# Optimization experiments

Measured on AMD Instinct MI355X. Metric: run time of the kernel, lower is better.

The kernel has to match this reference:

```python
import jax, jax.numpy as jnp
import numpy as np

B, S, E, H, F = 8, 1024, 1024, 16, 4096
D = E // H  # head_dim = 64
EPS = 1e-5


def setup_inputs() -> dict:
    key = jax.random.key(0)
    ks = jax.random.split(key, 12)
    s = 0.02
    return {
        "x": jax.random.normal(ks[0], (B, S, E), dtype=jnp.float32),
        # per-head projections (shared across heads), torch stores [out,in]; we use [in,out]
        "Wq": jax.random.normal(ks[1], (D, D), dtype=jnp.float32) * s,
        "Wk": jax.random.normal(ks[2], (D, D), dtype=jnp.float32) * s,
        "Wv": jax.random.normal(ks[3], (D, D), dtype=jnp.float32) * s,
        "Wo": jax.random.normal(ks[4], (E, E), dtype=jnp.float32) * s,
        "bo": jnp.zeros((E,), dtype=jnp.float32),
        "W1": jax.random.normal(ks[5], (E, F), dtype=jnp.float32) * s,
        "b1": jnp.zeros((F,), dtype=jnp.float32),
        "W2": jax.random.normal(ks[6], (F, E), dtype=jnp.float32) * s,
        "b2": jnp.zeros((E,), dtype=jnp.float32),
        "g1": jnp.ones((E,), dtype=jnp.float32),
        "beta1": jnp.zeros((E,), dtype=jnp.float32),
        "g2": jnp.ones((E,), dtype=jnp.float32),
        "beta2": jnp.zeros((E,), dtype=jnp.float32),
    }


def _layer_norm(x, g, b):
    m = jnp.mean(x, axis=-1, keepdims=True)
    v = jnp.mean(jnp.square(x - m), axis=-1, keepdims=True)
    return (x - m) * jax.lax.rsqrt(v + EPS) * g + b


def reference(x, Wq, Wk, Wv, Wo, bo, W1, b1, W2, b2, g1, beta1, g2, beta2):
    b, s, e = x.shape
    # --- attention sublayer (pre-norm) ---
    nx = _layer_norm(x, g1, beta1)
    h = nx.reshape(b, s, H, D)              # [B,S,H,D]
    q = h @ Wq                               # per-head linear, weight shared over heads
    k = h @ Wk
    v = h @ Wv
    energy = jnp.einsum('bqhd,bkhd->bhqk', q, k)  # full [B,H,S,S] scores
    mask = jnp.tril(jnp.ones((s, s), dtype=bool))
    energy = jnp.where(mask, energy, -jnp.inf)
    att = jax.nn.softmax(energy / jnp.sqrt(jnp.float32(e)), axis=-1)  # NOTE: scale by sqrt(embed_dim)
    o = jnp.einsum('bhqk,bkhd->bqhd', att, v).reshape(b, s, e)
    x = x + (o @ Wo + bo)
    # --- MLP sublayer (pre-norm); dropout is identity in eval ---
    nx = _layer_norm(x, g2, beta2)
    x = x + (jax.nn.relu(nx @ W1 + b1) @ W2 + b2)
    return x
```

## Files before the change

kernel.cpp:

```cpp
#include <hip/hip_runtime.h>

typedef unsigned short u16;
typedef __attribute__((ext_vector_type(4))) float f4;
typedef __attribute__((ext_vector_type(8))) short s8v;
typedef __attribute__((ext_vector_type(4))) unsigned short u16x4;

#define DEVINL __device__ __forceinline__

DEVINL float b2f(u16 u) { union { unsigned i; float f; } x; x.i = ((unsigned)u) << 16; return x.f; }
DEVINL u16 f2b(float f) {
  union { float f; unsigned i; } x; x.f = f;
  unsigned r = 0x7FFFu + ((x.i >> 16) & 1u);
  return (u16)((x.i + r) >> 16);
}

#define GLD_LDS16(g, l)                                                        \
  __builtin_amdgcn_global_load_lds((__attribute__((address_space(1))) void*)(g), \
                                   (__attribute__((address_space(3))) void*)(l), 16, 0, 0)

__global__ __launch_bounds__(256) void k_transpose(const float* __restrict__ in,
                                                   u16* __restrict__ out, int R, int C) {
  __shared__ float t[32][33];
  int tx = threadIdx.x & 31, ty = threadIdx.x >> 5;
  int c0 = blockIdx.x * 32, r0 = blockIdx.y * 32;
#pragma unroll
  for (int i = 0; i < 32; i += 8)
    t[ty + i][tx] = in[(long)(r0 + ty + i) * C + (c0 + tx)];
  __syncthreads();
#pragma unroll
  for (int i = 0; i < 32; i += 8)
    out[(long)(c0 + ty + i) * R + (r0 + tx)] = f2b(t[tx][ty + i]);
}

__global__ __launch_bounds__(256) void k_vtrans(const u16* __restrict__ v, u16* __restrict__ vt) {
  __shared__ u16 t[64][72];
  int bh = blockIdx.x, b = bh >> 4, h = bh & 15;
  int s0 = blockIdx.y * 64;
  int tid = threadIdx.x;
#pragma unroll
  for (int p = 0; p < 2; ++p) {
    int idx = p * 256 + tid;
    int sl = idx >> 3, c8 = (idx & 7) * 8;
    *(s8v*)(&t[sl][c8]) = *(const s8v*)(v + (((long)(b * 1024 + s0 + sl) * 16 + h) * 64) + c8);
  }
  __syncthreads();
#pragma unroll
  for (int p = 0; p < 2; ++p) {
    int idx = p * 256 + tid;
    int d = idx >> 3, c8 = (idx & 7) * 8;
    s8v o;
#pragma unroll
    for (int e = 0; e < 8; ++e) o[e] = (short)t[c8 + e][d];
    *(s8v*)(vt + ((long)bh * 64 + d) * 1024 + s0 + c8) = o;
  }
}

__global__ __launch_bounds__(256) void k_layernorm(const float* __restrict__ x,
                                                   const float* __restrict__ g,
                                                   const float* __restrict__ be,
                                                   u16* __restrict__ out) {
  long row = blockIdx.x;
  int tid = threadIdx.x;
  f4 v = ((const f4*)(x + row * 1024))[tid];
  float s = v[0] + v[1] + v[2] + v[3];
  float s2 = v[0] * v[0] + v[1] * v[1] + v[2] * v[2] + v[3] * v[3];
#pragma unroll
  for (int off = 32; off > 0; off >>= 1) {
    s += __shfl_down(s, off, 64);
    s2 += __shfl_down(s2, off, 64);
  }
  __shared__ float red[8];
  int wv = tid >> 6, ln = tid & 63;
  if (ln == 0) { red[wv] = s; red[4 + wv] = s2; }
  __syncthreads();
  s = red[0] + red[1] + red[2] + red[3];
  s2 = red[4] + red[5] + red[6] + red[7];
  float mean = s * (1.0f / 1024.0f);
  float var = s2 * (1.0f / 1024.0f) - mean * mean;
  float rs = rsqrtf(var + 1e-5f);
  f4 gg = ((const f4*)g)[tid];
  f4 bb = ((const f4*)be)[tid];
  u16x4 o;
#pragma unroll
  for (int i = 0; i < 4; ++i) o[i] = f2b((v[i] - mean) * rs * gg[i] + bb[i]);
  ((u16x4*)(out + row * 1024))[tid] = o;
}

__global__ __launch_bounds__(256) void k_qkv(const u16* __restrict__ nx, const u16* __restrict__ WqT,
                                             const u16* __restrict__ WkT, const u16* __restrict__ WvT,
                                             u16* __restrict__ q, u16* __restrict__ k,
                                             u16* __restrict__ v) {
  int tid = threadIdx.x, lane = tid & 63, wave = tid >> 6;
  int quad = lane >> 4, l16 = lane & 15;
  long rbase = (long)blockIdx.x * 64 + wave * 16;
  s8v a0 = *(const s8v*)(nx + (rbase + l16) * 64 + quad * 8);
  s8v a1 = *(const s8v*)(nx + (rbase + l16) * 64 + 32 + quad * 8);
  const u16* Ws[3] = {WqT, WkT, WvT};
  u16* Os[3] = {q, k, v};
#pragma unroll
  for (int t = 0; t < 3; ++t) {
#pragma unroll
    for (int j = 0; j < 4; ++j) {
      s8v b0 = *(const s8v*)(Ws[t] + (j * 16 + l16) * 64 + quad * 8);
      s8v b1 = *(const s8v*)(Ws[t] + (j * 16 + l16) * 64 + 32 + quad * 8);
      f4 acc = {0.f, 0.f, 0.f, 0.f};
      acc = __builtin_amdgcn_mfma_f32_16x16x32_bf16(a0, b0, acc, 0, 0, 0);
      acc = __builtin_amdgcn_mfma_f32_16x16x32_bf16(a1, b1, acc, 0, 0, 0);
#pragma unroll
      for (int r = 0; r < 4; ++r)
        Os[t][(rbase + quad * 4 + r) * 64 + j * 16 + l16] = f2b(acc[r]);
    }
  }
}

__global__ __launch_bounds__(256) void k_attn_mfma(const u16* __restrict__ q,
                                                   const u16* __restrict__ kk,
                                                   const u16* __restrict__ vt,
                                                   u16* __restrict__ o) {
  constexpr int LDK = 72;
  __shared__ u16 Ks[64 * LDK];
  __shared__ u16 Vt[64 * LDK];
  __shared__ u16 Ps[4][16 * LDK];
  int tid = threadIdx.x, lane = tid & 63, wave = tid >> 6;
  int quad = lane >> 4, l16 = lane & 15;
  int b = blockIdx.x >> 4, h = blockIdx.x & 15;
  int qi = (int)gridDim.y - 1 - (int)blockIdx.y;
  int q0 = qi * 64 + wave * 16;

  const u16* qp = q + (((long)(b * 1024 + q0 + l16)) * 16 + h) * 64;
  s8v aq0 = *(const s8v*)(qp + quad * 8);
  s8v aq1 = *(const s8v*)(qp + 32 + quad * 8);

  f4 O[4];
  float m_[4], l_[4];
#pragma unroll
  for (int jd = 0; jd < 4; ++jd) O[jd] = f4{0.f, 0.f, 0.f, 0.f};
#pragma unroll
  for (int r = 0; r < 4; ++r) { m_[r] = -__builtin_inff(); l_[r] = 0.f; }

  for (int kt = 0; kt <= qi; ++kt) {
    __syncthreads();
#pragma unroll
    for (int p = 0; p < 2; ++p) {
      int idx = p * 256 + tid;
      int row = idx >> 3, c8 = (idx & 7) * 8;
      *(s8v*)(Ks + row * LDK + c8) =
          *(const s8v*)(kk + (((long)(b * 1024 + kt * 64 + row)) * 16 + h) * 64 + c8);
      *(s8v*)(Vt + row * LDK + c8) =
          *(const s8v*)(vt + ((long)blockIdx.x * 64 + row) * 1024 + kt * 64 + c8);
    }
    __syncthreads();

    f4 sf[4];
#pragma unroll
    for (int jn = 0; jn < 4; ++jn) {
      s8v b0 = *(const s8v*)(Ks + (jn * 16 + l16) * LDK + quad * 8);
      s8v b1 = *(const s8v*)(Ks + (jn * 16 + l16) * LDK + 32 + quad * 8);
      f4 acc = f4{0.f, 0.f, 0.f, 0.f};
      acc = __builtin_amdgcn_mfma_f32_16x16x32_bf16(aq0, b0, acc, 0, 0, 0);
      acc = __builtin_amdgcn_mfma_f32_16x16x32_bf16(aq1, b1, acc, 0, 0, 0);
      sf[jn] = acc;
    }
    bool diag = (kt == qi);
    float rm[4];
#pragma unroll
    for (int r = 0; r < 4; ++r) rm[r] = -__builtin_inff();
#pragma unroll
    for (int jn = 0; jn < 4; ++jn)
#pragma unroll
      for (int r = 0; r < 4; ++r) {
        float v = sf[jn][r] * 0.03125f;
        if (diag && (jn * 16 + l16 > wave * 16 + quad * 4 + r)) v = -__builtin_inff();
        sf[jn][r] = v;
        rm[r] = fmaxf(rm[r], v);
      }
#pragma unroll
    for (int off = 1; off < 16; off <<= 1)
#pragma unroll
      for (int r = 0; r < 4; ++r) rm[r] = fmaxf(rm[r], __shfl_xor(rm[r], off, 64));
    float alpha[4], rs[4];
#pragma unroll
    for (int r = 0; r < 4; ++r) {
      float mn = fmaxf(m_[r], rm[r]);
      alpha[r] = __expf(m_[r] - mn);
      m_[r] = mn;
      rs[r] = 0.f;
    }
#pragma unroll
    for (int jn = 0; jn < 4; ++jn)
#pragma unroll
      for (int r = 0; r < 4; ++r) {
        float p = __expf(sf[jn][r] - m_[r]);
        rs[r] += p;
        Ps[wave][(quad * 4 + r) * LDK + jn * 16 + l16] = f2b(p);
      }
#pragma unroll
    for (int off = 1; off < 16; off <<= 1)
#pragma unroll
      for (int r = 0; r < 4; ++r) rs[r] += __shfl_xor(rs[r], off, 64);
#pragma unroll
    for (int r = 0; r < 4; ++r) l_[r] = l_[r] * alpha[r] + rs[r];
#pragma unroll
    for (int jd = 0; jd < 4; ++jd)
#pragma unroll
      for (int r = 0; r < 4; ++r) O[jd][r] *= alpha[r];
    asm volatile("s_waitcnt lgkmcnt(0)" ::: "memory");
    s8v p0 = *(const s8v*)(&Ps[wave][l16 * LDK + quad * 8]);
    s8v p1 = *(const s8v*)(&Ps[wave][l16 * LDK + 32 + quad * 8]);
#pragma unroll
    for (int jd = 0; jd < 4; ++jd) {
      s8v b0 = *(const s8v*)(Vt + (jd * 16 + l16) * LDK + quad * 8);
      s8v b1 = *(const s8v*)(Vt + (jd * 16 + l16) * LDK + 32 + quad * 8);
      O[jd] = __builtin_amdgcn_mfma_f32_16x16x32_bf16(p0, b0, O[jd], 0, 0, 0);
      O[jd] = __builtin_amdgcn_mfma_f32_16x16x32_bf16(p1, b1, O[jd], 0, 0, 0);
    }
  }
#pragma unroll
  for (int r = 0; r < 4; ++r) {
    float inv = 1.0f / l_[r];
    u16* op = o + (((long)(b * 1024 + q0 + quad * 4 + r)) * 16 + h) * 64;
#pragma unroll
    for (int jd = 0; jd < 4; ++jd) op[jd * 16 + l16] = f2b(O[jd][r] * inv);
  }
}

template <int EPI>
__global__ __launch_bounds__(256) void k_gemm_bt(const u16* __restrict__ A, const u16* __restrict__ BT,
                                                 const float* __restrict__ bias,
                                                 const float* __restrict__ resid,
                                                 void* __restrict__ outp, int M, int N, int K) {
  __shared__ u16 sA[2][128 * 32];
  __shared__ u16 sB[2][128 * 32];
  int tid = threadIdx.x, lane = tid & 63, wave = tid >> 6;
  int quad = lane >> 4, l16 = lane & 15;
  int wm = wave >> 1, wn = wave & 1;
  long bm = blockIdx.x, bn = blockIdx.y;
  int srow = tid >> 2, scol = (tid & 3) * 8;
  const u16* ga = A + (bm * 128 + srow) * (long)K + scol;
  const u16* gb = BT + (bn * 128 + srow) * (long)K + scol;
  int woff = wave * 1024;

  f4 acc[4][4];
#pragma unroll
  for (int i = 0; i < 4; ++i)
#pragma unroll
    for (int j = 0; j < 4; ++j) acc[i][j] = f4{0.f, 0.f, 0.f, 0.f};

  {
    char* lA = (char*)&sA[0][0] + woff;
    char* lB = (char*)&sB[0][0] + woff;
    GLD_LDS16(ga, lA);
    GLD_LDS16(ga + 64 * (long)K, lA + 4096);
    GLD_LDS16(gb, lB);
    GLD_LDS16(gb + 64 * (long)K, lB + 4096);
  }

  for (int k0 = 0; k0 < K; k0 += 32) {
    int cur = (k0 >> 5) & 1;
    __syncthreads();
    int k1 = k0 + 32;
    if (k1 < K) {
      char* lA = (char*)&sA[cur ^ 1][0] + woff;
      char* lB = (char*)&sB[cur ^ 1][0] + woff;
      GLD_LDS16(ga + k1, lA);
      GLD_LDS16(ga + 64 * (long)K + k1, lA + 4096);
      GLD_LDS16(gb + k1, lB);
      GLD_LDS16(gb + 64 * (long)K + k1, lB + 4096);
    }
    const u16* cA = sA[cur];
    const u16* cB = sB[cur];
    s8v aF[4], bF[4];
#pragma unroll
    for (int i = 0; i < 4; ++i)
      aF[i] = *(const s8v*)(cA + (wm * 64 + i * 16 + l16) * 32 + quad * 8);
#pragma unroll
    for (int j = 0; j < 4; ++j)
      bF[j] = *(const s8v*)(cB + (wn * 64 + j * 16 + l16) * 32 + quad * 8);
#pragma unroll
    for (int i = 0; i < 4; ++i)
#pragma unroll
      for (int j = 0; j < 4; ++j)
        acc[i][j] = __builtin_amdgcn_mfma_f32_16x16x32_bf16(aF[i], bF[j], acc[i][j], 0, 0, 0);
  }

#pragma unroll
  for (int i = 0; i < 4; ++i) {
#pragma unroll
    for (int j = 0; j < 4; ++j) {
      long row = bm * 128 + wm * 64 + i * 16 + quad * 4;
      int col = (int)bn * 128 + wn * 64 + j * 16 + l16;
      float bcol = bias[col];
#pragma unroll
      for (int r = 0; r < 4; ++r) {
        float val = acc[i][j][r] + bcol;
        if (EPI == 1) {
          ((u16*)outp)[(row + r) * (long)N + col] = f2b(val > 0.f ? val : 0.f);
        } else {
          ((float*)outp)[(row + r) * (long)N + col] = resid[(row + r) * (long)N + col] + val;
        }
      }
    }
  }
}

extern "C" void kernel_launch(void* const* d_in, const int* in_sizes, int n_in, void* d_out,
                              int out_size, void* d_ws, size_t ws_size, hipStream_t stream) {
  const float* x = (const float*)d_in[0];
  const float* Wq = (const float*)d_in[1];
  const float* Wk = (const float*)d_in[2];
  const float* Wv = (const float*)d_in[3];
  const float* Wo = (const float*)d_in[4];
  const float* bo = (const float*)d_in[5];
  const float* W1 = (const float*)d_in[6];
  const float* b1 = (const float*)d_in[7];
  const float* W2 = (const float*)d_in[8];
  const float* b2 = (const float*)d_in[9];
  const float* g1 = (const float*)d_in[10];
  const float* be1 = (const float*)d_in[11];
  const float* g2 = (const float*)d_in[12];
  const float* be2 = (const float*)d_in[13];

  char* ws = (char*)d_ws;
  const size_t MB = 1ull << 20;
  u16* nx = (u16*)(ws + 0);
  u16* qb = (u16*)(ws + 16 * MB);
  u16* kb = (u16*)(ws + 32 * MB);
  u16* vb = (u16*)(ws + 48 * MB);
  float* x1 = (float*)(ws + 64 * MB);
  u16* h1 = (u16*)(ws + 96 * MB);
  u16* vtr = (u16*)(ws + 96 * MB);
  u16* WoT = (u16*)(ws + 160 * MB);
  u16* W1T = (u16*)(ws + 162 * MB);
  u16* W2T = (u16*)(ws + 170 * MB);
  u16* WqT = (u16*)(ws + 178 * MB);
  u16* WkT = WqT + 64 * 64;
  u16* WvT = WkT + 64 * 64;
  u16* ob = nx;
  u16* nx2 = qb;

  k_transpose<<<dim3(32, 32), 256, 0, stream>>>(Wo, WoT, 1024, 1024);
  k_transpose<<<dim3(128, 32), 256, 0, stream>>>(W1, W1T, 1024, 4096);
  k_transpose<<<dim3(32, 128), 256, 0, stream>>>(W2, W2T, 4096, 1024);
  k_transpose<<<dim3(2, 2), 256, 0, stream>>>(Wq, WqT, 64, 64);
  k_transpose<<<dim3(2, 2), 256, 0, stream>>>(Wk, WkT, 64, 64);
  k_transpose<<<dim3(2, 2), 256, 0, stream>>>(Wv, WvT, 64, 64);

  k_layernorm<<<8192, 256, 0, stream>>>(x, g1, be1, nx);
  k_qkv<<<2048, 256, 0, stream>>>(nx, WqT, WkT, WvT, qb, kb, vb);
  k_vtrans<<<dim3(128, 16), 256, 0, stream>>>(vb, vtr);
  k_attn_mfma<<<dim3(128, 16), 256, 0, stream>>>(qb, kb, vtr, ob);
  k_gemm_bt<2><<<dim3(64, 8), 256, 0, stream>>>(ob, WoT, bo, x, x1, 8192, 1024, 1024);

  k_layernorm<<<8192, 256, 0, stream>>>(x1, g2, be2, nx2);
  k_gemm_bt<1><<<dim3(64, 32), 256, 0, stream>>>(nx2, W1T, b1, nullptr, h1, 8192, 4096, 1024);
  k_gemm_bt<2><<<dim3(64, 8), 256, 0, stream>>>(h1, W2T, b2, x1, d_out, 8192, 1024, 4096);
}
```

Baseline: 457.2 us.

## Split K across two wave groups per block for N=1024 GEMMs

Adds a 512-thread GEMM kernel in which two groups of four waves each handle half of the K dimension for the same 128x128 output tile. Their partial accumulators are summed through LDS before the bias and residual epilogue. It replaces the Wo and W2 projections, whose 512-block grids leave the GPU's CUs under-occupied with waves. The cost is double the LDS (64KB) and an extra reduction and sync step.

```diff
diff --git a/kernel.cpp b/kernel.cpp
--- a/kernel.cpp
+++ b/kernel.cpp
@@ -297,6 +297,97 @@
           ((u16*)outp)[(row + r) * (long)N + col] = f2b(val > 0.f ? val : 0.f);
         } else {
           ((float*)outp)[(row + r) * (long)N + col] = resid[(row + r) * (long)N + col] + val;
+        }
+      }
+    }
+  }
+}
+
+template <int EPI>
+__global__ __launch_bounds__(512) void k_gemm_sk(const u16* __restrict__ A, const u16* __restrict__ BT,
+                                                 const float* __restrict__ bias,
+                                                 const float* __restrict__ resid,
+                                                 void* __restrict__ outp, int M, int N, int K) {
+  __shared__ char smem[65536];
+  int tid = threadIdx.x;
+  int grp = tid >> 8, gt = tid & 255;
+  int lane = tid & 63, w4 = (tid >> 6) & 3;
+  int quad = lane >> 4, l16 = lane & 15;
+  int wm = w4 >> 1, wn = w4 & 1;
+  long bm = blockIdx.x, bn = blockIdx.y;
+  int srow = gt >> 2, scol = (gt & 3) * 8;
+  int Kh = K >> 1;
+  const u16* ga = A + (bm * 128 + srow) * (long)K + grp * Kh + scol;
+  const u16* gb = BT + (bn * 128 + srow) * (long)K + grp * Kh + scol;
+  char* aB[2] = {smem + (grp * 2 + 0) * 8192, smem + (grp * 2 + 1) * 8192};
+  char* bB[2] = {smem + 32768 + (grp * 2 + 0) * 8192, smem + 32768 + (grp * 2 + 1) * 8192};
+  int woff = w4 * 1024;
+
+  f4 acc[4][4];
+#pragma unroll
+  for (int i = 0; i < 4; ++i)
+#pragma unroll
+    for (int j = 0; j < 4; ++j) acc[i][j] = f4{0.f, 0.f, 0.f, 0.f};
+
+  {
+    GLD_LDS16(ga, aB[0] + woff);
+    GLD_LDS16(ga + 64 * (long)K, aB[0] + woff + 4096);
+    GLD_LDS16(gb, bB[0] + woff);
+    GLD_LDS16(gb + 64 * (long)K, bB[0] + woff + 4096);
+  }
+
+  for (int k0 = 0; k0 < Kh; k0 += 32) {
+    int cur = (k0 >> 5) & 1;
+    __syncthreads();
+    int k1 = k0 + 32;
+    if (k1 < Kh) {
+      GLD_LDS16(ga + k1, aB[cur ^ 1] + woff);
+      GLD_LDS16(ga + 64 * (long)K + k1, aB[cur ^ 1] + woff + 4096);
+      GLD_LDS16(gb + k1, bB[cur ^ 1] + woff);
+      GLD_LDS16(gb + 64 * (long)K + k1, bB[cur ^ 1] + woff + 4096);
+    }
+    const u16* cA = (const u16*)aB[cur];
+    const u16* cB = (const u16*)bB[cur];
+    s8v aF[4], bF[4];
+#pragma unroll
+    for (int i = 0; i < 4; ++i)
+      aF[i] = *(const s8v*)(cA + (wm * 64 + i * 16 + l16) * 32 + quad * 8);
+#pragma unroll
+    for (int j = 0; j < 4; ++j)
+      bF[j] = *(const s8v*)(cB + (wn * 64 + j * 16 + l16) * 32 + quad * 8);
+#pragma unroll
+    for (int i = 0; i < 4; ++i)
+#pragma unroll
+      for (int j = 0; j < 4; ++j)
+        acc[i][j] = __builtin_amdgcn_mfma_f32_16x16x32_bf16(aF[i], bF[j], acc[i][j], 0, 0, 0);
+  }
+
+  __syncthreads();
+  f4* red = (f4*)smem;
+  if (grp == 1) {
+#pragma unroll
+    for (int i = 0; i < 4; ++i)
+#pragma unroll
+      for (int j = 0; j < 4; ++j) red[w4 * 1024 + (i * 4 + j) * 64 + lane] = acc[i][j];
+  }
+  __syncthreads();
+  if (grp == 0) {
+#pragma unroll
+    for (int i = 0; i < 4; ++i) {
+#pragma unroll
+      for (int j = 0; j < 4; ++j) {
+        f4 other = red[w4 * 1024 + (i * 4 + j) * 64 + lane];
+        long row = bm * 128 + wm * 64 + i * 16 + quad * 4;
+        int col = (int)bn * 128 + wn * 64 + j * 16 + l16;
+        float bcol = bias[col];
+#pragma unroll
+        for (int r = 0; r < 4; ++r) {
+          float val = acc[i][j][r] + other[r] + bcol;
+          if (EPI == 1) {
+            ((u16*)outp)[(row + r) * (long)N + col] = f2b(val > 0.f ? val : 0.f);
+          } else {
+            ((float*)outp)[(row + r) * (long)N + col] = resid[(row + r) * (long)N + col] + val;
+          }
         }
       }
     }
@@ -349,9 +440,9 @@
   k_qkv<<<2048, 256, 0, stream>>>(nx, WqT, WkT, WvT, qb, kb, vb);
   k_vtrans<<<dim3(128, 16), 256, 0, stream>>>(vb, vtr);
   k_attn_mfma<<<dim3(128, 16), 256, 0, stream>>>(qb, kb, vtr, ob);
-  k_gemm_bt<2><<<dim3(64, 8), 256, 0, stream>>>(ob, WoT, bo, x, x1, 8192, 1024, 1024);
+  k_gemm_sk<2><<<dim3(64, 8), 512, 0, stream>>>(ob, WoT, bo, x, x1, 8192, 1024, 1024);
 
   k_layernorm<<<8192, 256, 0, stream>>>(x1, g2, be2, nx2);
   k_gemm_bt<1><<<dim3(64, 32), 256, 0, stream>>>(nx2, W1T, b1, nullptr, h1, 8192, 4096, 1024);
-  k_gemm_bt<2><<<dim3(64, 8), 256, 0, stream>>>(h1, W2T, b2, x1, d_out, 8192, 1024, 4096);
-}
+  k_gemm_sk<2><<<dim3(64, 8), 512, 0, stream>>>(h1, W2T, b2, x1, d_out, 8192, 1024, 4096);
+}
```

Result: slower. 487.7 us (+6.7%).
